# Optimization experiments

Hardware: AMD Instinct MI355X
Metric: run time of the kernel (lower is better)

The kernel has to match this reference:

```python
import jax, jax.numpy as jnp
import numpy as np

EMBED_DIM = 1024
NUM_HEADS = 16
HEAD_DIM = EMBED_DIM // NUM_HEADS


def setup_inputs() -> dict:
    key = jax.random.key(0)
    ks = jax.random.split(key, 11)
    Lq, N, E = 4096, 4, EMBED_DIM
    Lk = 4096
    s = 1.0 / np.sqrt(E)
    return {
        "q": jax.random.normal(ks[0], (Lq, N, E), jnp.float32),
        "k": jax.random.normal(ks[1], (Lk, N, E), jnp.float32),
        "v": jax.random.normal(ks[2], (Lk, N, E), jnp.float32),
        "Wq": jax.random.normal(ks[3], (E, E), jnp.float32) * s,
        "bq": jnp.zeros((E,), jnp.float32),
        "Wk": jax.random.normal(ks[4], (E, E), jnp.float32) * s,
        "bk": jnp.zeros((E,), jnp.float32),
        "Wv": jax.random.normal(ks[5], (E, E), jnp.float32) * s,
        "bv": jnp.zeros((E,), jnp.float32),
        "Wo": jax.random.normal(ks[6], (E, E), jnp.float32) * s,
        "bo": jnp.zeros((E,), jnp.float32),
    }


def reference(q, k, v, Wq, bq, Wk, bk, Wv, bv, Wo, bo):
    Lq, N, E = q.shape
    Lk = k.shape[0]
    H, D = NUM_HEADS, HEAD_DIM
    # Linear projections (torch Linear: x @ W.T + b)
    qp = q @ Wq.T + bq  # [Lq, N, E]
    kp = k @ Wk.T + bk  # [Lk, N, E]
    vp = v @ Wv.T + bv  # [Lk, N, E]
    # Split heads -> [N, H, L, D]
    qh = qp.reshape(Lq, N, H, D).transpose(1, 2, 0, 3)
    kh = kp.reshape(Lk, N, H, D).transpose(1, 2, 0, 3)
    vh = vp.reshape(Lk, N, H, D).transpose(1, 2, 0, 3)
    # Efficient (linear) attention
    kh = jax.nn.softmax(kh, axis=-2)            # softmax over sequence (L)
    v_prime = jnp.einsum('nhld,nhle->nhde', kh, vh)  # [N,H,D,D]
    qh = jax.nn.softmax(qh, axis=-1)            # softmax over feature (D)
    attn = jnp.einsum('nhld,nhde->nhle', qh, v_prime)  # [N,H,Lq,D]
    out = attn.transpose(2, 0, 1, 3).reshape(Lq, N, E)
    out = out @ Wo.T + bo
    return out
```

## Files before the change

### kernel.cpp

```cpp
#include <hip/hip_runtime.h>

typedef unsigned short u16;
typedef short s8v __attribute__((ext_vector_type(8)));
typedef float f4v __attribute__((ext_vector_type(4)));

#define D_LQ 4096
#define D_N 4
#define D_E 1024
#define D_M 16384
#define D_COLS 4096

__device__ __forceinline__ u16 f2b(float f) {
  unsigned u = __float_as_uint(f);
  return (u16)((u + 0x7FFFu + ((u >> 16) & 1u)) >> 16);
}
__device__ __forceinline__ float b2f(u16 x) {
  return __uint_as_float(((unsigned)x) << 16);
}
__device__ __forceinline__ s8v cvt8(float4 a, float4 b) {
  s8v o;
  o[0] = (short)f2b(a.x); o[1] = (short)f2b(a.y);
  o[2] = (short)f2b(a.z); o[3] = (short)f2b(a.w);
  o[4] = (short)f2b(b.x); o[5] = (short)f2b(b.y);
  o[6] = (short)f2b(b.z); o[7] = (short)f2b(b.w);
  return o;
}
__device__ __forceinline__ void gl_lds16(const void* g, void* l) {
  __builtin_amdgcn_global_load_lds(
      (const __attribute__((address_space(1))) void*)g,
      (__attribute__((address_space(3))) void*)l, 16, 0, 0);
}

__global__ void cvt_bf16(const float* __restrict__ in, u16* __restrict__ out, long n8) {
  long i = (long)blockIdx.x * 256 + threadIdx.x;
  if (i >= n8) return;
  const float4* p = (const float4*)in + 2 * i;
  float4 a = p[0], b = p[1];
  *(s8v*)(out + i * 8) = cvt8(a, b);
}

__global__ void cvt_w4(const float* __restrict__ W0, const float* __restrict__ W1,
                       const float* __restrict__ W2, const float* __restrict__ W3,
                       u16* __restrict__ O0, u16* __restrict__ O1,
                       u16* __restrict__ O2, u16* __restrict__ O3) {
  long i = (long)blockIdx.x * 256 + threadIdx.x;
  int w = blockIdx.y;
  const float* W = (w == 0) ? W0 : (w == 1) ? W1 : (w == 2) ? W2 : W3;
  u16* O = (w == 0) ? O0 : (w == 1) ? O1 : (w == 2) ? O2 : O3;
  const float4* p = (const float4*)W + 2 * i;
  float4 a = p[0], b = p[1];
  *(s8v*)(O + i * 8) = cvt8(a, b);
}

__global__ __launch_bounds__(256)
void gemm_bf(const u16* __restrict__ A, const u16* __restrict__ B,
             const float* __restrict__ bias, float* __restrict__ C) {
  __shared__ u16 As[128 * 32];
  __shared__ u16 Bs[128 * 32];
  const int tid = threadIdx.x;
  const int lane = tid & 63, r15 = lane & 15, khi = lane >> 4;
  const int wave = tid >> 6, wm = wave >> 1, wn = wave & 1;
  const int wg = blockIdx.y * 8 + blockIdx.x;
  const int xcd = wg & 7, j = wg >> 3;
  const int by = xcd * 16 + (j >> 3);
  const int bx = j & 7;
  f4v acc[4][4] = {};
  const u16* a0 = A + (long)(by * 128 + (tid >> 2)) * D_E + (tid & 3) * 8;
  const u16* b0 = B + (long)(bx * 128 + (tid >> 2)) * D_E + (tid & 3) * 8;
  const long rstep = (long)64 * D_E;
  u16* lA = As + tid * 8;
  u16* lB = Bs + tid * 8;
  for (int kt = 0; kt < D_E; kt += 32) {
    __syncthreads();
    gl_lds16(a0 + kt, lA);
    gl_lds16(a0 + rstep + kt, lA + 2048);
    gl_lds16(b0 + kt, lB);
    gl_lds16(b0 + rstep + kt, lB + 2048);
    __syncthreads();
    s8v af[4], bf[4];
#pragma unroll
    for (int m = 0; m < 4; m++)
      af[m] = *(const s8v*)(As + (wm * 64 + m * 16 + r15) * 32 + khi * 8);
#pragma unroll
    for (int n = 0; n < 4; n++)
      bf[n] = *(const s8v*)(Bs + (wn * 64 + n * 16 + r15) * 32 + khi * 8);
#pragma unroll
    for (int m = 0; m < 4; m++)
#pragma unroll
      for (int n = 0; n < 4; n++)
        acc[m][n] = __builtin_amdgcn_mfma_f32_16x16x32_bf16(af[m], bf[n], acc[m][n], 0, 0, 0);
  }
#pragma unroll
  for (int m = 0; m < 4; m++) {
    const int row = by * 128 + wm * 64 + m * 16 + khi * 4;
#pragma unroll
    for (int n = 0; n < 4; n++) {
      const int col = bx * 128 + wn * 64 + n * 16 + r15;
      const float bb = bias[col];
#pragma unroll
      for (int j2 = 0; j2 < 4; j2++)
        C[(long)(row + j2) * D_E + col] = acc[m][n][j2] + bb;
    }
  }
}

__global__ __launch_bounds__(256)
void gemm_bfb(const u16* __restrict__ A, const u16* __restrict__ B,
              const float* __restrict__ bias, u16* __restrict__ C) {
  __shared__ u16 As[128 * 32];
  __shared__ u16 Bs[128 * 32];
  const int tid = threadIdx.x;
  const int lane = tid & 63, r15 = lane & 15, khi = lane >> 4;
  const int wave = tid >> 6, wm = wave >> 1, wn = wave & 1;
  const int wg = blockIdx.y * 8 + blockIdx.x;
  const int xcd = wg & 7, j = wg >> 3;
  const int by = xcd * 16 + (j >> 3);
  const int bx = j & 7;
  f4v acc[4][4] = {};
  const u16* a0 = A + (long)(by * 128 + (tid >> 2)) * D_E + (tid & 3) * 8;
  const u16* b0 = B + (long)(bx * 128 + (tid >> 2)) * D_E + (tid & 3) * 8;
  const long rstep = (long)64 * D_E;
  u16* lA = As + tid * 8;
  u16* lB = Bs + tid * 8;
  for (int kt = 0; kt < D_E; kt += 32) {
    __syncthreads();
    gl_lds16(a0 + kt, lA);
    gl_lds16(a0 + rstep + kt, lA + 2048);
    gl_lds16(b0 + kt, lB);
    gl_lds16(b0 + rstep + kt, lB + 2048);
    __syncthreads();
    s8v af[4], bf[4];
#pragma unroll
    for (int m = 0; m < 4; m++)
      af[m] = *(const s8v*)(As + (wm * 64 + m * 16 + r15) * 32 + khi * 8);
#pragma unroll
    for (int n = 0; n < 4; n++)
      bf[n] = *(const s8v*)(Bs + (wn * 64 + n * 16 + r15) * 32 + khi * 8);
#pragma unroll
    for (int m = 0; m < 4; m++)
#pragma unroll
      for (int n = 0; n < 4; n++)
        acc[m][n] = __builtin_amdgcn_mfma_f32_16x16x32_bf16(af[m], bf[n], acc[m][n], 0, 0, 0);
  }
#pragma unroll
  for (int m = 0; m < 4; m++) {
    const int row = by * 128 + wm * 64 + m * 16 + khi * 4;
#pragma unroll
    for (int n = 0; n < 4; n++) {
      const int col = bx * 128 + wn * 64 + n * 16 + r15;
      const float bb = bias[col];
#pragma unroll
      for (int j2 = 0; j2 < 4; j2++)
        C[(long)(row + j2) * D_E + col] = f2b(acc[m][n][j2] + bb);
    }
  }
}

__global__ __launch_bounds__(256)
void gemm_bf_qsm(const u16* __restrict__ A, const u16* __restrict__ B,
                 const float* __restrict__ bias, u16* __restrict__ Csm) {
  __shared__ u16 As[128 * 32];
  __shared__ u16 Bs[128 * 32];
  const int tid = threadIdx.x;
  const int lane = tid & 63, r15 = lane & 15, khi = lane >> 4;
  const int wave = tid >> 6, wm = wave >> 1, wn = wave & 1;
  const int wg = blockIdx.y * 8 + blockIdx.x;
  const int xcd = wg & 7, j = wg >> 3;
  const int by = xcd * 16 + (j >> 3);
  const int bx = j & 7;
  f4v acc[4][4] = {};
  const u16* a0 = A + (long)(by * 128 + (tid >> 2)) * D_E + (tid & 3) * 8;
  const u16* b0 = B + (long)(bx * 128 + (tid >> 2)) * D_E + (tid & 3) * 8;
  const long rstep = (long)64 * D_E;
  u16* lA = As + tid * 8;
  u16* lB = Bs + tid * 8;
  for (int kt = 0; kt < D_E; kt += 32) {
    __syncthreads();
    gl_lds16(a0 + kt, lA);
    gl_lds16(a0 + rstep + kt, lA + 2048);
    gl_lds16(b0 + kt, lB);
    gl_lds16(b0 + rstep + kt, lB + 2048);
    __syncthreads();
    s8v af[4], bf[4];
#pragma unroll
    for (int m = 0; m < 4; m++)
      af[m] = *(const s8v*)(As + (wm * 64 + m * 16 + r15) * 32 + khi * 8);
#pragma unroll
    for (int n = 0; n < 4; n++)
      bf[n] = *(const s8v*)(Bs + (wn * 64 + n * 16 + r15) * 32 + khi * 8);
#pragma unroll
    for (int m = 0; m < 4; m++)
#pragma unroll
      for (int n = 0; n < 4; n++)
        acc[m][n] = __builtin_amdgcn_mfma_f32_16x16x32_bf16(af[m], bf[n], acc[m][n], 0, 0, 0);
  }
  const int colb = bx * 128 + wn * 64;
  float bb[4];
#pragma unroll
  for (int n = 0; n < 4; n++) bb[n] = bias[colb + n * 16 + r15];
#pragma unroll
  for (int m = 0; m < 4; m++) {
    const int row = by * 128 + wm * 64 + m * 16 + khi * 4;
#pragma unroll
    for (int j2 = 0; j2 < 4; j2++) {
      float e[4], s = 0.f;
#pragma unroll
      for (int n = 0; n < 4; n++) { e[n] = __expf(acc[m][n][j2] + bb[n]); s += e[n]; }
      s += __shfl_xor(s, 1);
      s += __shfl_xor(s, 2);
      s += __shfl_xor(s, 4);
      s += __shfl_xor(s, 8);
      float rs = 1.f / s;
#pragma unroll
      for (int n = 0; n < 4; n++)
        Csm[(long)(row + j2) * D_E + colb + n * 16 + r15] = f2b(e[n] * rs);
    }
  }
}

__global__ void k_sum(const u16* __restrict__ kb, float* __restrict__ psum) {
  int col = blockIdx.x * 256 + threadIdx.x;
  const u16* p = kb + (long)blockIdx.y * 64 * D_COLS + col;
  float s = 0.f;
  for (int l = 0; l < 64; l++) s += __expf(b2f(p[(long)l * D_COLS]));
  psum[blockIdx.y * D_COLS + col] = s;
}

__global__ void k_combine(const float* __restrict__ psum, float* __restrict__ crs) {
  int col = blockIdx.x * 256 + threadIdx.x;
  float s = 0.f;
  for (int i = 0; i < 64; i++) s += psum[i * D_COLS + col];
  crs[col] = 1.f / s;
}

__global__ __launch_bounds__(256)
void vprime_part(const u16* __restrict__ kw, const u16* __restrict__ vp,
                 const float* __restrict__ crs, float* __restrict__ part) {
  __shared__ float Ks[64 * 64];
  __shared__ float Vs[64 * 64];
  __shared__ float crS[64];
  int g = blockIdx.x, lc = blockIdx.y;
  int n = g >> 4, h = g & 15;
  int tid = threadIdx.x;
  int dt = (tid >> 4) * 4, et = (tid & 15) * 4;
  int r = tid >> 2, c16 = (tid & 3) * 16;
  if (tid < 64) crS[tid] = crs[n * D_E + h * 64 + tid];
  float acc[4][4] = {};
  long base = (long)lc * 512 * D_COLS + n * D_E + h * 64;
  for (int ch = 0; ch < 8; ch++) {
    long off = base + (long)(ch * 64 + r) * D_COLS + c16;
    __syncthreads();
#pragma unroll
    for (int qq = 0; qq < 16; qq++) {
      Ks[r * 64 + c16 + qq] = __expf(b2f(kw[off + qq])) * crS[c16 + qq];
      Vs[r * 64 + c16 + qq] = b2f(vp[off + qq]);
    }
    __syncthreads();
    for (int l = 0; l < 64; l++) {
      float kf[4], vf[4];
#pragma unroll
      for (int i = 0; i < 4; i++) { kf[i] = Ks[l * 64 + dt + i]; vf[i] = Vs[l * 64 + et + i]; }
#pragma unroll
      for (int i = 0; i < 4; i++)
#pragma unroll
        for (int j = 0; j < 4; j++) acc[i][j] += kf[i] * vf[j];
    }
  }
#pragma unroll
  for (int i = 0; i < 4; i++)
#pragma unroll
    for (int j = 0; j < 4; j++)
      part[(((long)lc * 64 + g) * 64 + (dt + i)) * 64 + et + j] = acc[i][j];
}

__global__ void vprime_red(const float* __restrict__ part, u16* __restrict__ vpT) {
  long id = (long)blockIdx.x * 256 + threadIdx.x;
  float s = 0.f;
  for (int lc = 0; lc < 8; lc++) s += part[(long)lc * 64 * 4096 + id];
  long g = id >> 12, d = (id >> 6) & 63, e = id & 63;
  vpT[(g << 12) + e * 64 + d] = f2b(s);
}

__global__ __launch_bounds__(256)
void attn_mfma(const u16* __restrict__ qsm, const u16* __restrict__ vpT,
               u16* __restrict__ attn) {
  __shared__ u16 Qs[128 * 64];
  __shared__ u16 Ps[64 * 64];
  const int lt = blockIdx.x, g = blockIdx.y;
  const int nb = g >> 4, h = g & 15;
  const int tid = threadIdx.x;
  const int lane = tid & 63, r15 = lane & 15, khi = lane >> 4;
  const int w = tid >> 6;
#pragma unroll
  for (int it = 0; it < 4; it++) {
    int c = it * 256 + tid;
    int row = c >> 3, cb = (c & 7) * 16;
    int swz = cb ^ ((row & 7) << 4);
    long rg = (long)(lt * 128 + row) * 4 + nb;
    gl_lds16(qsm + rg * D_E + h * 64 + (swz >> 1), Qs + c * 8);
  }
#pragma unroll
  for (int it = 0; it < 2; it++) {
    int c = it * 256 + tid;
    int row = c >> 3, cb = (c & 7) * 16;
    int swz = cb ^ ((row & 7) << 4);
    gl_lds16(vpT + ((long)g << 12) + row * 64 + (swz >> 1), Ps + c * 8);
  }
  __syncthreads();
  f4v acc[2][4] = {};
#pragma unroll
  for (int ks = 0; ks < 2; ks++) {
    s8v af[2], bf[4];
#pragma unroll
    for (int mf = 0; mf < 2; mf++) {
      int row = w * 32 + mf * 16 + r15;
      int boff = row * 128 + ((ks * 64 + khi * 16) ^ ((row & 7) << 4));
      af[mf] = *(const s8v*)((const char*)Qs + boff);
    }
#pragma unroll
    for (int nf = 0; nf < 4; nf++) {
      int row = nf * 16 + r15;
      int boff = row * 128 + ((ks * 64 + khi * 16) ^ ((row & 7) << 4));
      bf[nf] = *(const s8v*)((const char*)Ps + boff);
    }
#pragma unroll
    for (int mf = 0; mf < 2; mf++)
#pragma unroll
      for (int nf = 0; nf < 4; nf++)
        acc[mf][nf] = __builtin_amdgcn_mfma_f32_16x16x32_bf16(af[mf], bf[nf], acc[mf][nf], 0, 0, 0);
  }
#pragma unroll
  for (int mf = 0; mf < 2; mf++) {
#pragma unroll
    for (int nf = 0; nf < 4; nf++) {
#pragma unroll
      for (int j = 0; j < 4; j++) {
        int rl = w * 32 + mf * 16 + khi * 4 + j;
        long rg = (long)(lt * 128 + rl) * 4 + nb;
        attn[rg * D_E + h * 64 + nf * 16 + r15] = f2b(acc[mf][nf][j]);
      }
    }
  }
}

__global__ void sentinel(float* __restrict__ out, int wsbad) {
  if (blockIdx.x == 0 && threadIdx.x == 0 && wsbad) {
    out[0] += 100.0f;
  }
}

extern "C" void kernel_launch(void* const* d_in, const int* in_sizes, int n_in,
                              void* d_out, int out_size, void* d_ws, size_t ws_size,
                              hipStream_t stream) {
  const float* q  = (const float*)d_in[0];
  const float* k  = (const float*)d_in[1];
  const float* v  = (const float*)d_in[2];
  const float* Wq = (const float*)d_in[3];
  const float* bq = (const float*)d_in[4];
  const float* Wk = (const float*)d_in[5];
  const float* bk = (const float*)d_in[6];
  const float* Wv = (const float*)d_in[7];
  const float* bv = (const float*)d_in[8];
  const float* Wo = (const float*)d_in[9];
  const float* bo = (const float*)d_in[10];

  char* ws = (char*)d_ws;
  size_t off = 0;
  u16* kb; u16* vb; float* psum; float* crs; float* part; u16* vpT;
  u16* xb; u16* Wqb; u16* Wkb; u16* Wvb; u16* Wob;
  kb   = (u16*)(ws + off);   off += (size_t)D_M * D_E * 2;
  vb   = (u16*)(ws + off);   off += (size_t)D_M * D_E * 2;
  psum = (float*)(ws + off); off += (size_t)64 * D_COLS * 4;
  crs  = (float*)(ws + off); off += (size_t)D_COLS * 4;
  part = (float*)(ws + off); off += (size_t)8 * 64 * 4096 * 4;
  vpT  = (u16*)(ws + off);   off += (size_t)64 * 4096 * 2;
  xb   = (u16*)(ws + off);   off += (size_t)D_M * D_E * 2;
  Wqb  = (u16*)(ws + off);   off += (size_t)D_E * D_E * 2;
  Wkb  = (u16*)(ws + off);   off += (size_t)D_E * D_E * 2;
  Wvb  = (u16*)(ws + off);   off += (size_t)D_E * D_E * 2;
  Wob  = (u16*)(ws + off);   off += (size_t)D_E * D_E * 2;
  size_t need = off;
  u16* qsm = kb;
  int wsbad = (ws_size < need) ? 1 : 0;

  const long nX8 = (long)D_M * D_E / 8;
  const long nW8 = (long)D_E * D_E / 8;
  dim3 blk(256);
  dim3 ggrid(D_E / 128, D_M / 128);

  cvt_w4<<<dim3(nW8 / 256, 4), blk, 0, stream>>>(Wq, Wk, Wv, Wo, Wqb, Wkb, Wvb, Wob);

  cvt_bf16<<<dim3(nX8 / 256), blk, 0, stream>>>(k, xb, nX8);
  gemm_bfb<<<ggrid, blk, 0, stream>>>(xb, Wkb, bk, kb);
  cvt_bf16<<<dim3(nX8 / 256), blk, 0, stream>>>(v, xb, nX8);
  gemm_bfb<<<ggrid, blk, 0, stream>>>(xb, Wvb, bv, vb);

  k_sum<<<dim3(16, 64), blk, 0, stream>>>(kb, psum);
  k_combine<<<dim3(16), blk, 0, stream>>>(psum, crs);

  vprime_part<<<dim3(64, 8), blk, 0, stream>>>(kb, vb, crs, part);
  vprime_red<<<dim3(64 * 4096 / 256), blk, 0, stream>>>(part, vpT);

  cvt_bf16<<<dim3(nX8 / 256), blk, 0, stream>>>(q, xb, nX8);
  gemm_bf_qsm<<<ggrid, blk, 0, stream>>>(xb, Wqb, bq, qsm);

  attn_mfma<<<dim3(32, 64), blk, 0, stream>>>(qsm, vpT, xb);

  gemm_bf<<<ggrid, blk, 0, stream>>>(xb, Wob, bo, (float*)d_out);

  sentinel<<<dim3(1), dim3(64), 0, stream>>>((float*)d_out, wsbad);
}
```

Before: 335.8 us.

## Fold v_prime into Wo per batch and load fp32 activations directly in GEMMs

Precomputes U[n] = Wo·blockdiag(v_prime[n]) per batch with a small MFMA kernel, so softmaxed Q feeds straight into a batched output GEMM. This drops the separate attention kernel and its intermediate buffer. Separately, the K and Q projection GEMMs now read fp32 inputs into LDS through an XOR-swizzled layout and convert them to bf16 in registers, which removes two standalone conversion passes. In exchange the GEMMs move twice as many bytes for A into LDS, and the folded Ub matrix is rounded to bf16, which changes numerics.

```diff
diff --git a/kernel.cpp b/kernel.cpp
--- a/kernel.cpp
+++ b/kernel.cpp
@@ -3,6 +3,7 @@
 typedef unsigned short u16;
 typedef short s8v __attribute__((ext_vector_type(8)));
 typedef float f4v __attribute__((ext_vector_type(4)));
+typedef unsigned u4v __attribute__((ext_vector_type(4)));
 
 #define D_LQ 4096
 #define D_N 4
@@ -24,6 +25,15 @@
   o[4] = (short)f2b(b.x); o[5] = (short)f2b(b.y);
   o[6] = (short)f2b(b.z); o[7] = (short)f2b(b.w);
   return o;
+}
+__device__ __forceinline__ s8v cvtfrag(f4v a, f4v b) {
+  unsigned r0, r1, r2, r3;
+  asm("v_cvt_pk_bf16_f32 %0, %1, %2" : "=v"(r0) : "v"(a[0]), "v"(a[1]));
+  asm("v_cvt_pk_bf16_f32 %0, %1, %2" : "=v"(r1) : "v"(a[2]), "v"(a[3]));
+  asm("v_cvt_pk_bf16_f32 %0, %1, %2" : "=v"(r2) : "v"(b[0]), "v"(b[1]));
+  asm("v_cvt_pk_bf16_f32 %0, %1, %2" : "=v"(r3) : "v"(b[2]), "v"(b[3]));
+  u4v t = {r0, r1, r2, r3};
+  return __builtin_bit_cast(s8v, t);
 }
 __device__ __forceinline__ void gl_lds16(const void* g, void* l) {
   __builtin_amdgcn_global_load_lds(
@@ -50,58 +60,6 @@
   const float4* p = (const float4*)W + 2 * i;
   float4 a = p[0], b = p[1];
   *(s8v*)(O + i * 8) = cvt8(a, b);
-}
-
-__global__ __launch_bounds__(256)
-void gemm_bf(const u16* __restrict__ A, const u16* __restrict__ B,
-             const float* __restrict__ bias, float* __restrict__ C) {
-  __shared__ u16 As[128 * 32];
-  __shared__ u16 Bs[128 * 32];
-  const int tid = threadIdx.x;
-  const int lane = tid & 63, r15 = lane & 15, khi = lane >> 4;
-  const int wave = tid >> 6, wm = wave >> 1, wn = wave & 1;
-  const int wg = blockIdx.y * 8 + blockIdx.x;
-  const int xcd = wg & 7, j = wg >> 3;
-  const int by = xcd * 16 + (j >> 3);
-  const int bx = j & 7;
-  f4v acc[4][4] = {};
-  const u16* a0 = A + (long)(by * 128 + (tid >> 2)) * D_E + (tid & 3) * 8;
-  const u16* b0 = B + (long)(bx * 128 + (tid >> 2)) * D_E + (tid & 3) * 8;
-  const long rstep = (long)64 * D_E;
-  u16* lA = As + tid * 8;
-  u16* lB = Bs + tid * 8;
-  for (int kt = 0; kt < D_E; kt += 32) {
-    __syncthreads();
-    gl_lds16(a0 + kt, lA);
-    gl_lds16(a0 + rstep + kt, lA + 2048);
-    gl_lds16(b0 + kt, lB);
-    gl_lds16(b0 + rstep + kt, lB + 2048);
-    __syncthreads();
-    s8v af[4], bf[4];
-#pragma unroll
-    for (int m = 0; m < 4; m++)
-      af[m] = *(const s8v*)(As + (wm * 64 + m * 16 + r15) * 32 + khi * 8);
-#pragma unroll
-    for (int n = 0; n < 4; n++)
-      bf[n] = *(const s8v*)(Bs + (wn * 64 + n * 16 + r15) * 32 + khi * 8);
-#pragma unroll
-    for (int m = 0; m < 4; m++)
-#pragma unroll
-      for (int n = 0; n < 4; n++)
-        acc[m][n] = __builtin_amdgcn_mfma_f32_16x16x32_bf16(af[m], bf[n], acc[m][n], 0, 0, 0);
-  }
-#pragma unroll
-  for (int m = 0; m < 4; m++) {
-    const int row = by * 128 + wm * 64 + m * 16 + khi * 4;
-#pragma unroll
-    for (int n = 0; n < 4; n++) {
-      const int col = bx * 128 + wn * 64 + n * 16 + r15;
-      const float bb = bias[col];
-#pragma unroll
-      for (int j2 = 0; j2 < 4; j2++)
-        C[(long)(row + j2) * D_E + col] = acc[m][n][j2] + bb;
-    }
-  }
 }
 
 __global__ __launch_bounds__(256)
@@ -157,9 +115,9 @@
 }
 
 __global__ __launch_bounds__(256)
-void gemm_bf_qsm(const u16* __restrict__ A, const u16* __restrict__ B,
-                 const float* __restrict__ bias, u16* __restrict__ Csm) {
-  __shared__ u16 As[128 * 32];
+void gemm_bfb_f32a(const float* __restrict__ A, const u16* __restrict__ B,
+                   const float* __restrict__ bias, u16* __restrict__ C) {
+  __shared__ float Asf[128 * 32];
   __shared__ u16 Bs[128 * 32];
   const int tid = threadIdx.x;
   const int lane = tid & 63, r15 = lane & 15, khi = lane >> 4;
@@ -169,22 +127,88 @@
   const int by = xcd * 16 + (j >> 3);
   const int bx = j & 7;
   f4v acc[4][4] = {};
-  const u16* a0 = A + (long)(by * 128 + (tid >> 2)) * D_E + (tid & 3) * 8;
   const u16* b0 = B + (long)(bx * 128 + (tid >> 2)) * D_E + (tid & 3) * 8;
   const long rstep = (long)64 * D_E;
-  u16* lA = As + tid * 8;
   u16* lB = Bs + tid * 8;
   for (int kt = 0; kt < D_E; kt += 32) {
     __syncthreads();
-    gl_lds16(a0 + kt, lA);
-    gl_lds16(a0 + rstep + kt, lA + 2048);
+#pragma unroll
+    for (int it = 0; it < 4; it++) {
+      int c = it * 256 + tid;
+      int row = c >> 3;
+      int scb = (c & 7) ^ (row & 7);
+      gl_lds16(A + (long)(by * 128 + row) * D_E + kt + scb * 4, Asf + c * 4);
+    }
     gl_lds16(b0 + kt, lB);
     gl_lds16(b0 + rstep + kt, lB + 2048);
     __syncthreads();
     s8v af[4], bf[4];
 #pragma unroll
-    for (int m = 0; m < 4; m++)
-      af[m] = *(const s8v*)(As + (wm * 64 + m * 16 + r15) * 32 + khi * 8);
+    for (int m = 0; m < 4; m++) {
+      int rr = wm * 64 + m * 16 + r15;
+      f4v x0 = *(const f4v*)(Asf + rr * 32 + (((khi * 2) ^ (rr & 7)) * 4));
+      f4v x1 = *(const f4v*)(Asf + rr * 32 + (((khi * 2 + 1) ^ (rr & 7)) * 4));
+      af[m] = cvtfrag(x0, x1);
+    }
+#pragma unroll
+    for (int n = 0; n < 4; n++)
+      bf[n] = *(const s8v*)(Bs + (wn * 64 + n * 16 + r15) * 32 + khi * 8);
+#pragma unroll
+    for (int m = 0; m < 4; m++)
+#pragma unroll
+      for (int n = 0; n < 4; n++)
+        acc[m][n] = __builtin_amdgcn_mfma_f32_16x16x32_bf16(af[m], bf[n], acc[m][n], 0, 0, 0);
+  }
+#pragma unroll
+  for (int m = 0; m < 4; m++) {
+    const int row = by * 128 + wm * 64 + m * 16 + khi * 4;
+#pragma unroll
+    for (int n = 0; n < 4; n++) {
+      const int col = bx * 128 + wn * 64 + n * 16 + r15;
+      const float bb = bias[col];
+#pragma unroll
+      for (int j2 = 0; j2 < 4; j2++)
+        C[(long)(row + j2) * D_E + col] = f2b(acc[m][n][j2] + bb);
+    }
+  }
+}
+
+__global__ __launch_bounds__(256)
+void gemm_qsm_f32a(const float* __restrict__ A, const u16* __restrict__ B,
+                   const float* __restrict__ bias, u16* __restrict__ Csm) {
+  __shared__ float Asf[128 * 32];
+  __shared__ u16 Bs[128 * 32];
+  const int tid = threadIdx.x;
+  const int lane = tid & 63, r15 = lane & 15, khi = lane >> 4;
+  const int wave = tid >> 6, wm = wave >> 1, wn = wave & 1;
+  const int wg = blockIdx.y * 8 + blockIdx.x;
+  const int xcd = wg & 7, j = wg >> 3;
+  const int by = xcd * 16 + (j >> 3);
+  const int bx = j & 7;
+  f4v acc[4][4] = {};
+  const u16* b0 = B + (long)(bx * 128 + (tid >> 2)) * D_E + (tid & 3) * 8;
+  const long rstep = (long)64 * D_E;
+  u16* lB = Bs + tid * 8;
+  for (int kt = 0; kt < D_E; kt += 32) {
+    __syncthreads();
+#pragma unroll
+    for (int it = 0; it < 4; it++) {
+      int c = it * 256 + tid;
+      int row = c >> 3;
+      int scb = (c & 7) ^ (row & 7);
+      gl_lds16(A + (long)(by * 128 + row) * D_E + kt + scb * 4, Asf + c * 4);
+    }
+    gl_lds16(b0 + kt, lB);
+    gl_lds16(b0 + rstep + kt, lB + 2048);
+    __syncthreads();
+    s8v af[4], bf[4];
+#pragma unroll
+    for (int m = 0; m < 4; m++) {
+      int rr = wm * 64 + m * 16 + r15;
+      f4v x0 = *(const f4v*)(Asf + rr * 32 + (((khi * 2) ^ (rr & 7)) * 4));
+      f4v x1 = *(const f4v*)(Asf + rr * 32 + (((khi * 2 + 1) ^ (rr & 7)) * 4));
+      af[m] = cvtfrag(x0, x1);
+    }
 #pragma unroll
     for (int n = 0; n < 4; n++)
       bf[n] = *(const s8v*)(Bs + (wn * 64 + n * 16 + r15) * 32 + khi * 8);
@@ -273,20 +297,19 @@
       part[(((long)lc * 64 + g) * 64 + (dt + i)) * 64 + et + j] = acc[i][j];
 }
 
-__global__ void vprime_red(const float* __restrict__ part, u16* __restrict__ vpT) {
+__global__ void vprime_red(const float* __restrict__ part, u16* __restrict__ vpb) {
   long id = (long)blockIdx.x * 256 + threadIdx.x;
   float s = 0.f;
   for (int lc = 0; lc < 8; lc++) s += part[(long)lc * 64 * 4096 + id];
-  long g = id >> 12, d = (id >> 6) & 63, e = id & 63;
-  vpT[(g << 12) + e * 64 + d] = f2b(s);
-}
-
-__global__ __launch_bounds__(256)
-void attn_mfma(const u16* __restrict__ qsm, const u16* __restrict__ vpT,
-               u16* __restrict__ attn) {
+  vpb[id] = f2b(s);
+}
+
+__global__ __launch_bounds__(256)
+void u_mfma(const u16* __restrict__ Wob, const u16* __restrict__ vpb,
+            u16* __restrict__ Ub) {
   __shared__ u16 Qs[128 * 64];
   __shared__ u16 Ps[64 * 64];
-  const int lt = blockIdx.x, g = blockIdx.y;
+  const int ot = blockIdx.x, g = blockIdx.y;
   const int nb = g >> 4, h = g & 15;
   const int tid = threadIdx.x;
   const int lane = tid & 63, r15 = lane & 15, khi = lane >> 4;
@@ -296,15 +319,14 @@
     int c = it * 256 + tid;
     int row = c >> 3, cb = (c & 7) * 16;
     int swz = cb ^ ((row & 7) << 4);
-    long rg = (long)(lt * 128 + row) * 4 + nb;
-    gl_lds16(qsm + rg * D_E + h * 64 + (swz >> 1), Qs + c * 8);
+    gl_lds16(Wob + (long)(ot * 128 + row) * D_E + h * 64 + (swz >> 1), Qs + c * 8);
   }
 #pragma unroll
   for (int it = 0; it < 2; it++) {
     int c = it * 256 + tid;
     int row = c >> 3, cb = (c & 7) * 16;
     int swz = cb ^ ((row & 7) << 4);
-    gl_lds16(vpT + ((long)g << 12) + row * 64 + (swz >> 1), Ps + c * 8);
+    gl_lds16(vpb + ((long)g << 12) + row * 64 + (swz >> 1), Ps + c * 8);
   }
   __syncthreads();
   f4v acc[2][4] = {};
@@ -335,10 +357,64 @@
     for (int nf = 0; nf < 4; nf++) {
 #pragma unroll
       for (int j = 0; j < 4; j++) {
-        int rl = w * 32 + mf * 16 + khi * 4 + j;
-        long rg = (long)(lt * 128 + rl) * 4 + nb;
-        attn[rg * D_E + h * 64 + nf * 16 + r15] = f2b(acc[mf][nf][j]);
+        int o = ot * 128 + w * 32 + mf * 16 + khi * 4 + j;
+        int d = nf * 16 + r15;
+        Ub[((long)nb * 1024 + o) * 1024 + h * 64 + d] = f2b(acc[mf][nf][j]);
       }
+    }
+  }
+}
+
+__global__ __launch_bounds__(256)
+void gemm_out(const u16* __restrict__ Aq, const u16* __restrict__ Bu,
+              const float* __restrict__ bias, float* __restrict__ C) {
+  __shared__ u16 As[128 * 32];
+  __shared__ u16 Bs[128 * 32];
+  const int tid = threadIdx.x;
+  const int lane = tid & 63, r15 = lane & 15, khi = lane >> 4;
+  const int wave = tid >> 6, wm = wave >> 1, wn = wave & 1;
+  const int n = blockIdx.z;
+  const int wg = blockIdx.y * 8 + blockIdx.x;
+  const int xcd = wg & 7, j = wg >> 3;
+  const int by = xcd * 4 + (j >> 3);
+  const int bx = j & 7;
+  f4v acc[4][4] = {};
+  const u16* a0 = Aq + ((long)(by * 128 + (tid >> 2)) * 4 + n) * D_E + (tid & 3) * 8;
+  const u16* b0 = Bu + ((long)n * 1024 + bx * 128 + (tid >> 2)) * D_E + (tid & 3) * 8;
+  const long rstepA = (long)64 * 4 * D_E;
+  const long rstepB = (long)64 * D_E;
+  u16* lA = As + tid * 8;
+  u16* lB = Bs + tid * 8;
+  for (int kt = 0; kt < D_E; kt += 32) {
+    __syncthreads();
+    gl_lds16(a0 + kt, lA);
+    gl_lds16(a0 + rstepA + kt, lA + 2048);
+    gl_lds16(b0 + kt, lB);
+    gl_lds16(b0 + rstepB + kt, lB + 2048);
+    __syncthreads();
+    s8v af[4], bf[4];
+#pragma unroll
+    for (int m = 0; m < 4; m++)
+      af[m] = *(const s8v*)(As + (wm * 64 + m * 16 + r15) * 32 + khi * 8);
+#pragma unroll
+    for (int nn = 0; nn < 4; nn++)
+      bf[nn] = *(const s8v*)(Bs + (wn * 64 + nn * 16 + r15) * 32 + khi * 8);
+#pragma unroll
+    for (int m = 0; m < 4; m++)
+#pragma unroll
+      for (int nn = 0; nn < 4; nn++)
+        acc[m][nn] = __builtin_amdgcn_mfma_f32_16x16x32_bf16(af[m], bf[nn], acc[m][nn], 0, 0, 0);
+  }
+#pragma unroll
+  for (int m = 0; m < 4; m++) {
+    const int row = by * 128 + wm * 64 + m * 16 + khi * 4;
+#pragma unroll
+    for (int nn = 0; nn < 4; nn++) {
+      const int col = bx * 128 + wn * 64 + nn * 16 + r15;
+      const float bb = bias[col];
+#pragma unroll
+      for (int j2 = 0; j2 < 4; j2++)
+        C[((long)(row + j2) * 4 + n) * D_E + col] = acc[m][nn][j2] + bb;
     }
   }
 }
@@ -366,19 +442,20 @@
 
   char* ws = (char*)d_ws;
   size_t off = 0;
-  u16* kb; u16* vb; float* psum; float* crs; float* part; u16* vpT;
-  u16* xb; u16* Wqb; u16* Wkb; u16* Wvb; u16* Wob;
+  u16* kb; u16* vb; float* psum; float* crs; float* part; u16* vpb;
+  u16* xb; u16* Wqb; u16* Wkb; u16* Wvb; u16* Wob; u16* Ub;
   kb   = (u16*)(ws + off);   off += (size_t)D_M * D_E * 2;
   vb   = (u16*)(ws + off);   off += (size_t)D_M * D_E * 2;
   psum = (float*)(ws + off); off += (size_t)64 * D_COLS * 4;
   crs  = (float*)(ws + off); off += (size_t)D_COLS * 4;
   part = (float*)(ws + off); off += (size_t)8 * 64 * 4096 * 4;
-  vpT  = (u16*)(ws + off);   off += (size_t)64 * 4096 * 2;
+  vpb  = (u16*)(ws + off);   off += (size_t)64 * 4096 * 2;
   xb   = (u16*)(ws + off);   off += (size_t)D_M * D_E * 2;
   Wqb  = (u16*)(ws + off);   off += (size_t)D_E * D_E * 2;
   Wkb  = (u16*)(ws + off);   off += (size_t)D_E * D_E * 2;
   Wvb  = (u16*)(ws + off);   off += (size_t)D_E * D_E * 2;
   Wob  = (u16*)(ws + off);   off += (size_t)D_E * D_E * 2;
+  Ub   = (u16*)(ws + off);   off += (size_t)4 * 1024 * 1024 * 2;
   size_t need = off;
   u16* qsm = kb;
   int wsbad = (ws_size < need) ? 1 : 0;
@@ -390,8 +467,7 @@
 
   cvt_w4<<<dim3(nW8 / 256, 4), blk, 0, stream>>>(Wq, Wk, Wv, Wo, Wqb, Wkb, Wvb, Wob);
 
-  cvt_bf16<<<dim3(nX8 / 256), blk, 0, stream>>>(k, xb, nX8);
-  gemm_bfb<<<ggrid, blk, 0, stream>>>(xb, Wkb, bk, kb);
+  gemm_bfb_f32a<<<ggrid, blk, 0, stream>>>(k, Wkb, bk, kb);
   cvt_bf16<<<dim3(nX8 / 256), blk, 0, stream>>>(v, xb, nX8);
   gemm_bfb<<<ggrid, blk, 0, stream>>>(xb, Wvb, bv, vb);
 
@@ -399,14 +475,13 @@
   k_combine<<<dim3(16), blk, 0, stream>>>(psum, crs);
 
   vprime_part<<<dim3(64, 8), blk, 0, stream>>>(kb, vb, crs, part);
-  vprime_red<<<dim3(64 * 4096 / 256), blk, 0, stream>>>(part, vpT);
-
-  cvt_bf16<<<dim3(nX8 / 256), blk, 0, stream>>>(q, xb, nX8);
-  gemm_bf_qsm<<<ggrid, blk, 0, stream>>>(xb, Wqb, bq, qsm);
-
-  attn_mfma<<<dim3(32, 64), blk, 0, stream>>>(qsm, vpT, xb);
-
-  gemm_bf<<<ggrid, blk, 0, stream>>>(xb, Wob, bo, (float*)d_out);
+  vprime_red<<<dim3(64 * 4096 / 256), blk, 0, stream>>>(part, vpb);
+
+  u_mfma<<<dim3(8, 64), blk, 0, stream>>>(Wob, vpb, Ub);
+
+  gemm_qsm_f32a<<<ggrid, blk, 0, stream>>>(q, Wqb, bq, qsm);
+
+  gemm_out<<<dim3(8, 32, 4), blk, 0, stream>>>(qsm, Ub, bo, (float*)d_out);
 
   sentinel<<<dim3(1), dim3(64), 0, stream>>>((float*)d_out, wsbad);
 }
```

After: 368.2 us. 1.1x slower.

## Fold per-head v_prime into output projection weights, removing attention kernel

Applied to the files above, without the earlier changes.

Computes, for each batch, a fused weight U = Wo_head · v_primeᵀ (sized 4×1024×1024) with a small MFMA kernel. The output GEMM then multiplies the softmaxed Q directly by U per batch. This drops the attention kernel and its bf16 intermediate round-trip through memory. It adds a small per-batch weight build and one more bf16 rounding of the combined product.

```diff
diff --git a/kernel.cpp b/kernel.cpp
--- a/kernel.cpp
+++ b/kernel.cpp
@@ -50,58 +50,6 @@
   const float4* p = (const float4*)W + 2 * i;
   float4 a = p[0], b = p[1];
   *(s8v*)(O + i * 8) = cvt8(a, b);
-}
-
-__global__ __launch_bounds__(256)
-void gemm_bf(const u16* __restrict__ A, const u16* __restrict__ B,
-             const float* __restrict__ bias, float* __restrict__ C) {
-  __shared__ u16 As[128 * 32];
-  __shared__ u16 Bs[128 * 32];
-  const int tid = threadIdx.x;
-  const int lane = tid & 63, r15 = lane & 15, khi = lane >> 4;
-  const int wave = tid >> 6, wm = wave >> 1, wn = wave & 1;
-  const int wg = blockIdx.y * 8 + blockIdx.x;
-  const int xcd = wg & 7, j = wg >> 3;
-  const int by = xcd * 16 + (j >> 3);
-  const int bx = j & 7;
-  f4v acc[4][4] = {};
-  const u16* a0 = A + (long)(by * 128 + (tid >> 2)) * D_E + (tid & 3) * 8;
-  const u16* b0 = B + (long)(bx * 128 + (tid >> 2)) * D_E + (tid & 3) * 8;
-  const long rstep = (long)64 * D_E;
-  u16* lA = As + tid * 8;
-  u16* lB = Bs + tid * 8;
-  for (int kt = 0; kt < D_E; kt += 32) {
-    __syncthreads();
-    gl_lds16(a0 + kt, lA);
-    gl_lds16(a0 + rstep + kt, lA + 2048);
-    gl_lds16(b0 + kt, lB);
-    gl_lds16(b0 + rstep + kt, lB + 2048);
-    __syncthreads();
-    s8v af[4], bf[4];
-#pragma unroll
-    for (int m = 0; m < 4; m++)
-      af[m] = *(const s8v*)(As + (wm * 64 + m * 16 + r15) * 32 + khi * 8);
-#pragma unroll
-    for (int n = 0; n < 4; n++)
-      bf[n] = *(const s8v*)(Bs + (wn * 64 + n * 16 + r15) * 32 + khi * 8);
-#pragma unroll
-    for (int m = 0; m < 4; m++)
-#pragma unroll
-      for (int n = 0; n < 4; n++)
-        acc[m][n] = __builtin_amdgcn_mfma_f32_16x16x32_bf16(af[m], bf[n], acc[m][n], 0, 0, 0);
-  }
-#pragma unroll
-  for (int m = 0; m < 4; m++) {
-    const int row = by * 128 + wm * 64 + m * 16 + khi * 4;
-#pragma unroll
-    for (int n = 0; n < 4; n++) {
-      const int col = bx * 128 + wn * 64 + n * 16 + r15;
-      const float bb = bias[col];
-#pragma unroll
-      for (int j2 = 0; j2 < 4; j2++)
-        C[(long)(row + j2) * D_E + col] = acc[m][n][j2] + bb;
-    }
-  }
 }
 
 __global__ __launch_bounds__(256)
@@ -273,20 +221,19 @@
       part[(((long)lc * 64 + g) * 64 + (dt + i)) * 64 + et + j] = acc[i][j];
 }
 
-__global__ void vprime_red(const float* __restrict__ part, u16* __restrict__ vpT) {
+__global__ void vprime_red(const float* __restrict__ part, u16* __restrict__ vpb) {
   long id = (long)blockIdx.x * 256 + threadIdx.x;
   float s = 0.f;
   for (int lc = 0; lc < 8; lc++) s += part[(long)lc * 64 * 4096 + id];
-  long g = id >> 12, d = (id >> 6) & 63, e = id & 63;
-  vpT[(g << 12) + e * 64 + d] = f2b(s);
+  vpb[id] = f2b(s);
 }
 
 __global__ __launch_bounds__(256)
-void attn_mfma(const u16* __restrict__ qsm, const u16* __restrict__ vpT,
-               u16* __restrict__ attn) {
+void u_mfma(const u16* __restrict__ Wob, const u16* __restrict__ vpb,
+            u16* __restrict__ Ub) {
   __shared__ u16 Qs[128 * 64];
   __shared__ u16 Ps[64 * 64];
-  const int lt = blockIdx.x, g = blockIdx.y;
+  const int ot = blockIdx.x, g = blockIdx.y;
   const int nb = g >> 4, h = g & 15;
   const int tid = threadIdx.x;
   const int lane = tid & 63, r15 = lane & 15, khi = lane >> 4;
@@ -296,15 +243,14 @@
     int c = it * 256 + tid;
     int row = c >> 3, cb = (c & 7) * 16;
     int swz = cb ^ ((row & 7) << 4);
-    long rg = (long)(lt * 128 + row) * 4 + nb;
-    gl_lds16(qsm + rg * D_E + h * 64 + (swz >> 1), Qs + c * 8);
+    gl_lds16(Wob + (long)(ot * 128 + row) * D_E + h * 64 + (swz >> 1), Qs + c * 8);
   }
 #pragma unroll
   for (int it = 0; it < 2; it++) {
     int c = it * 256 + tid;
     int row = c >> 3, cb = (c & 7) * 16;
     int swz = cb ^ ((row & 7) << 4);
-    gl_lds16(vpT + ((long)g << 12) + row * 64 + (swz >> 1), Ps + c * 8);
+    gl_lds16(vpb + ((long)g << 12) + row * 64 + (swz >> 1), Ps + c * 8);
   }
   __syncthreads();
   f4v acc[2][4] = {};
@@ -335,10 +281,64 @@
     for (int nf = 0; nf < 4; nf++) {
 #pragma unroll
       for (int j = 0; j < 4; j++) {
-        int rl = w * 32 + mf * 16 + khi * 4 + j;
-        long rg = (long)(lt * 128 + rl) * 4 + nb;
-        attn[rg * D_E + h * 64 + nf * 16 + r15] = f2b(acc[mf][nf][j]);
+        int o = ot * 128 + w * 32 + mf * 16 + khi * 4 + j;
+        int d = nf * 16 + r15;
+        Ub[((long)nb * 1024 + o) * 1024 + h * 64 + d] = f2b(acc[mf][nf][j]);
       }
+    }
+  }
+}
+
+__global__ __launch_bounds__(256)
+void gemm_out(const u16* __restrict__ Aq, const u16* __restrict__ Bu,
+              const float* __restrict__ bias, float* __restrict__ C) {
+  __shared__ u16 As[128 * 32];
+  __shared__ u16 Bs[128 * 32];
+  const int tid = threadIdx.x;
+  const int lane = tid & 63, r15 = lane & 15, khi = lane >> 4;
+  const int wave = tid >> 6, wm = wave >> 1, wn = wave & 1;
+  const int n = blockIdx.z;
+  const int wg = blockIdx.y * 8 + blockIdx.x;
+  const int xcd = wg & 7, j = wg >> 3;
+  const int by = xcd * 4 + (j >> 3);
+  const int bx = j & 7;
+  f4v acc[4][4] = {};
+  const u16* a0 = Aq + ((long)(by * 128 + (tid >> 2)) * 4 + n) * D_E + (tid & 3) * 8;
+  const u16* b0 = Bu + ((long)n * 1024 + bx * 128 + (tid >> 2)) * D_E + (tid & 3) * 8;
+  const long rstepA = (long)64 * 4 * D_E;
+  const long rstepB = (long)64 * D_E;
+  u16* lA = As + tid * 8;
+  u16* lB = Bs + tid * 8;
+  for (int kt = 0; kt < D_E; kt += 32) {
+    __syncthreads();
+    gl_lds16(a0 + kt, lA);
+    gl_lds16(a0 + rstepA + kt, lA + 2048);
+    gl_lds16(b0 + kt, lB);
+    gl_lds16(b0 + rstepB + kt, lB + 2048);
+    __syncthreads();
+    s8v af[4], bf[4];
+#pragma unroll
+    for (int m = 0; m < 4; m++)
+      af[m] = *(const s8v*)(As + (wm * 64 + m * 16 + r15) * 32 + khi * 8);
+#pragma unroll
+    for (int nn = 0; nn < 4; nn++)
+      bf[nn] = *(const s8v*)(Bs + (wn * 64 + nn * 16 + r15) * 32 + khi * 8);
+#pragma unroll
+    for (int m = 0; m < 4; m++)
+#pragma unroll
+      for (int nn = 0; nn < 4; nn++)
+        acc[m][nn] = __builtin_amdgcn_mfma_f32_16x16x32_bf16(af[m], bf[nn], acc[m][nn], 0, 0, 0);
+  }
+#pragma unroll
+  for (int m = 0; m < 4; m++) {
+    const int row = by * 128 + wm * 64 + m * 16 + khi * 4;
+#pragma unroll
+    for (int nn = 0; nn < 4; nn++) {
+      const int col = bx * 128 + wn * 64 + nn * 16 + r15;
+      const float bb = bias[col];
+#pragma unroll
+      for (int j2 = 0; j2 < 4; j2++)
+        C[((long)(row + j2) * 4 + n) * D_E + col] = acc[m][nn][j2] + bb;
     }
   }
 }
@@ -366,19 +366,20 @@
 
   char* ws = (char*)d_ws;
   size_t off = 0;
-  u16* kb; u16* vb; float* psum; float* crs; float* part; u16* vpT;
-  u16* xb; u16* Wqb; u16* Wkb; u16* Wvb; u16* Wob;
+  u16* kb; u16* vb; float* psum; float* crs; float* part; u16* vpb;
+  u16* xb; u16* Wqb; u16* Wkb; u16* Wvb; u16* Wob; u16* Ub;
   kb   = (u16*)(ws + off);   off += (size_t)D_M * D_E * 2;
   vb   = (u16*)(ws + off);   off += (size_t)D_M * D_E * 2;
   psum = (float*)(ws + off); off += (size_t)64 * D_COLS * 4;
   crs  = (float*)(ws + off); off += (size_t)D_COLS * 4;
   part = (float*)(ws + off); off += (size_t)8 * 64 * 4096 * 4;
-  vpT  = (u16*)(ws + off);   off += (size_t)64 * 4096 * 2;
+  vpb  = (u16*)(ws + off);   off += (size_t)64 * 4096 * 2;
   xb   = (u16*)(ws + off);   off += (size_t)D_M * D_E * 2;
   Wqb  = (u16*)(ws + off);   off += (size_t)D_E * D_E * 2;
   Wkb  = (u16*)(ws + off);   off += (size_t)D_E * D_E * 2;
   Wvb  = (u16*)(ws + off);   off += (size_t)D_E * D_E * 2;
   Wob  = (u16*)(ws + off);   off += (size_t)D_E * D_E * 2;
+  Ub   = (u16*)(ws + off);   off += (size_t)4 * 1024 * 1024 * 2;
   size_t need = off;
   u16* qsm = kb;
   int wsbad = (ws_size < need) ? 1 : 0;
@@ -399,14 +400,14 @@
   k_combine<<<dim3(16), blk, 0, stream>>>(psum, crs);
 
   vprime_part<<<dim3(64, 8), blk, 0, stream>>>(kb, vb, crs, part);
-  vprime_red<<<dim3(64 * 4096 / 256), blk, 0, stream>>>(part, vpT);
+  vprime_red<<<dim3(64 * 4096 / 256), blk, 0, stream>>>(part, vpb);
+
+  u_mfma<<<dim3(8, 64), blk, 0, stream>>>(Wob, vpb, Ub);
 
   cvt_bf16<<<dim3(nX8 / 256), blk, 0, stream>>>(q, xb, nX8);
   gemm_bf_qsm<<<ggrid, blk, 0, stream>>>(xb, Wqb, bq, qsm);
 
-  attn_mfma<<<dim3(32, 64), blk, 0, stream>>>(qsm, vpT, xb);
-
-  gemm_bf<<<ggrid, blk, 0, stream>>>(xb, Wob, bo, (float*)d_out);
+  gemm_out<<<dim3(8, 32, 4), blk, 0, stream>>>(qsm, Ub, bo, (float*)d_out);
 
   sentinel<<<dim3(1), dim3(64), 0, stream>>>((float*)d_out, wsbad);
 }
```

Measured after the change: 325.6 us. 3.1% less time.
